# Kernel tuning notes

Hardware: AMD Instinct MI355X
Metric: run time of the kernel (lower is better)

## Reference

```python
import jax, jax.numpy as jnp
import numpy as np

B, S, D, H, F = 2, 4096, 768, 12, 3072
DK = D // H
EPS = 1e-5


def _layernorm(x, alpha, gamma):
    # Faithful to the custom Layernormalization: torch.std (unbiased, ddof=1),
    # (x - mean) / (std + eps), scalar alpha/gamma.
    m = jnp.mean(x, axis=-1, keepdims=True)
    s = jnp.std(x, axis=-1, ddof=1, keepdims=True)
    return alpha * ((x - m) / (s + EPS)) + gamma


def setup_inputs() -> dict:
    key = jax.random.key(0)
    ks = jax.random.split(key, 12)
    sc = 0.02
    inp = {
        "x": jax.random.normal(ks[0], (B, S, D), jnp.float32),
        # attention projections, stored as [in, out]
        "wq": jax.random.normal(ks[1], (D, D), jnp.float32) * sc,
        "bq": jnp.zeros((D,), jnp.float32),
        "wk": jax.random.normal(ks[2], (D, D), jnp.float32) * sc,
        "bk": jnp.zeros((D,), jnp.float32),
        "wv": jax.random.normal(ks[3], (D, D), jnp.float32) * sc,
        "bv": jnp.zeros((D,), jnp.float32),
        "wo": jax.random.normal(ks[4], (D, D), jnp.float32) * sc,
        "bo": jnp.zeros((D,), jnp.float32),
        # feedforward
        "w1": jax.random.normal(ks[5], (D, F), jnp.float32) * sc,
        "b1": jnp.zeros((F,), jnp.float32),
        "w2": jax.random.normal(ks[6], (F, D), jnp.float32) * sc,
        "b2": jnp.zeros((D,), jnp.float32),
        # two residual LayerNorms, scalar params (alpha=1, gamma=0 at init)
        "a1": jnp.ones((1,), jnp.float32),
        "g1": jnp.zeros((1,), jnp.float32),
        "a2": jnp.ones((1,), jnp.float32),
        "g2": jnp.zeros((1,), jnp.float32),
    }
    return inp


def reference(x, wq, bq, wk, bk, wv, bv, wo, bo, w1, b1, w2, b2, a1, g1, a2, g2):
    # --- self attention sublayer ---
    q = (x @ wq + bq).reshape(B, S, H, DK).transpose(0, 2, 1, 3)  # [B,H,S,dk]
    k = (x @ wk + bk).reshape(B, S, H, DK).transpose(0, 2, 1, 3)
    v = (x @ wv + bv).reshape(B, S, H, DK).transpose(0, 2, 1, 3)
    scores = jnp.einsum("bhqd,bhkd->bhqk", q, k) / np.sqrt(DK).astype(np.float32)
    attn = jax.nn.softmax(scores, axis=-1)  # dropout is identity (p=0 / eval)
    ctx = jnp.einsum("bhqk,bhkd->bhqd", attn, v)  # [B,H,S,dk]
    ctx = ctx.transpose(0, 2, 1, 3).reshape(B, S, D)
    attn_out = ctx @ wo + bo
    x = _layernorm(x + attn_out, a1, g1)
    # --- feedforward sublayer ---
    ff = jax.nn.relu(x @ w1 + b1) @ w2 + b2
    x = _layernorm(x + ff, a2, g2)
    return x
```

## Files before the change

kernel.cpp:

```cpp
#include <hip/hip_runtime.h>
#include <hip/hip_bf16.h>
#include <cstdint>
#include <cstddef>

typedef unsigned short u16;
typedef __attribute__((ext_vector_type(8))) __bf16 bf16x8;
typedef __attribute__((ext_vector_type(4))) float f32x4;

#define AS1 __attribute__((address_space(1)))
#define AS3 __attribute__((address_space(3)))

__device__ __forceinline__ u16 f2bf(float f) {
    union { float f; uint32_t u; } v; v.f = f;
    uint32_t r = (v.u + 0x7FFFu + ((v.u >> 16) & 1u)) >> 16;
    return (u16)r;
}

__device__ __forceinline__ float bf2f(u16 b) {
    union { uint32_t u; float f; } v; v.u = ((uint32_t)b) << 16;
    return v.f;
}

__device__ __forceinline__ uint32_t pack_bf2(float lo, float hi) {
    __hip_bfloat162 p = __float22bfloat162_rn(float2{lo, hi});
    union { __hip_bfloat162 b; uint32_t u; } v; v.b = p;
    return v.u;
}

__device__ __forceinline__ f32x4 mfma16(bf16x8 a, bf16x8 b, f32x4 c) {
    return __builtin_amdgcn_mfma_f32_16x16x32_bf16(a, b, c, 0, 0, 0);
}

__device__ __forceinline__ void async16(const u16* g, u16* lds_uniform_base) {
    __builtin_amdgcn_global_load_lds((const AS1 void*)g, (AS3 void*)lds_uniform_base, 16, 0, 0);
}

__global__ __launch_bounds__(256)
void k_prep(const float* __restrict__ x, u16* __restrict__ xb,
            const float* __restrict__ wq, const float* __restrict__ wk,
            const float* __restrict__ wv, const float* __restrict__ wo,
            const float* __restrict__ w1, const float* __restrict__ w2,
            u16* __restrict__ wqkvt, u16* __restrict__ wot,
            u16* __restrict__ w1t, u16* __restrict__ w2t)
{
    int bx = blockIdx.x;
    if (bx < 6144) {
        int i = (bx * 256 + threadIdx.x) * 4;
        float4 f = *(const float4*)(x + i);
        xb[i + 0] = f2bf(f.x); xb[i + 1] = f2bf(f.y);
        xb[i + 2] = f2bf(f.z); xb[i + 3] = f2bf(f.w);
        return;
    }
    int t = bx - 6144;
    const float* in; u16* out; int R, C;
    if (t < 2304) {
        int m = t / 576; t -= m * 576;
        R = 768; C = 768;
        in = (m == 0) ? wq : (m == 1) ? wk : (m == 2) ? wv : wo;
        out = (m < 3) ? wqkvt + (size_t)m * 768 * 768 : wot;
    } else if (t < 4608) {
        t -= 2304; in = w1; out = w1t; R = 768; C = 3072;
    } else {
        t -= 4608; in = w2; out = w2t; R = 3072; C = 768;
    }
    int tilesX = C >> 5;
    int c0 = (t % tilesX) * 32, r0 = (t / tilesX) * 32;
    __shared__ float tile[32][33];
    int tx = threadIdx.x & 31, ty = threadIdx.x >> 5;
    #pragma unroll
    for (int i = ty; i < 32; i += 8)
        tile[i][tx] = in[(size_t)(r0 + i) * C + c0 + tx];
    __syncthreads();
    #pragma unroll
    for (int i = ty; i < 32; i += 8)
        out[(size_t)(c0 + i) * R + r0 + tx] = f2bf(tile[tx][i]);
}

template <bool RELU>
__global__ __launch_bounds__(256)
void k_gemm(const u16* __restrict__ A, const u16* __restrict__ Bt,
            const float* __restrict__ bias, u16* __restrict__ Cb,
            int M, int N, int K)
{
    __shared__ __align__(16) u16 lA[128 * 32];
    __shared__ __align__(16) u16 lB[128 * 32];
    const int tid = threadIdx.x;
    const int w = tid >> 6, lane = tid & 63;
    const int quad = lane >> 4, l15 = lane & 15;
    const int m0 = blockIdx.x * 128, n0 = blockIdx.y * 128;
    const int wm = (w >> 1) * 64, wn = (w & 1) * 64;
    const int sw = (quad ^ ((l15 >> 1) & 3)) * 8;

    const f32x4 fz = {0.f, 0.f, 0.f, 0.f};
    f32x4 acc[4][4];
    #pragma unroll
    for (int i = 0; i < 4; ++i)
        #pragma unroll
        for (int j = 0; j < 4; ++j) acc[i][j] = fz;

    for (int k0 = 0; k0 < K; k0 += 32) {
        #pragma unroll
        for (int r = 0; r < 2; ++r) {
            int c = r * 256 + tid;
            int row = c >> 2, ch = (c & 3) ^ ((row >> 1) & 3);
            async16(A + (size_t)(m0 + row) * K + k0 + ch * 8,
                    (u16*)lA + (size_t)(r * 256 + w * 64) * 8);
            async16(Bt + (size_t)(n0 + row) * K + k0 + ch * 8,
                    (u16*)lB + (size_t)(r * 256 + w * 64) * 8);
        }
        __syncthreads();
        bf16x8 af[4], bfr[4];
        #pragma unroll
        for (int i = 0; i < 4; ++i)
            af[i] = *(const bf16x8*)&lA[(wm + i * 16 + l15) * 32 + sw];
        #pragma unroll
        for (int j = 0; j < 4; ++j)
            bfr[j] = *(const bf16x8*)&lB[(wn + j * 16 + l15) * 32 + sw];
        #pragma unroll
        for (int i = 0; i < 4; ++i)
            #pragma unroll
            for (int j = 0; j < 4; ++j)
                acc[i][j] = mfma16(af[i], bfr[j], acc[i][j]);
        __syncthreads();
    }
    #pragma unroll
    for (int j = 0; j < 4; ++j) {
        int col = n0 + wn + j * 16 + l15;
        float bv = bias[col];
        #pragma unroll
        for (int i = 0; i < 4; ++i) {
            int row = m0 + wm + i * 16 + quad * 4;
            #pragma unroll
            for (int r = 0; r < 4; ++r) {
                float t = acc[i][j][r] + bv;
                if (RELU) t = fmaxf(t, 0.f);
                Cb[(size_t)(row + r) * N + col] = f2bf(t);
            }
        }
    }
}

__global__ __launch_bounds__(256)
void k_gemm_part(const u16* __restrict__ A, const u16* __restrict__ Bt,
                 float* __restrict__ C0, float* __restrict__ C1,
                 int M, int N, int K, int Kh)
{
    __shared__ __align__(16) u16 lA[128 * 32];
    __shared__ __align__(16) u16 lB[128 * 32];
    const int tid = threadIdx.x;
    const int w = tid >> 6, lane = tid & 63;
    const int quad = lane >> 4, l15 = lane & 15;
    const int m0 = blockIdx.x * 128, n0 = blockIdx.y * 128;
    const int wm = (w >> 1) * 64, wn = (w & 1) * 64;
    const int sw = (quad ^ ((l15 >> 1) & 3)) * 8;
    const int kbeg = blockIdx.z * Kh, kend = kbeg + Kh;
    float* __restrict__ C = blockIdx.z ? C1 : C0;

    const f32x4 fz = {0.f, 0.f, 0.f, 0.f};
    f32x4 acc[4][4];
    #pragma unroll
    for (int i = 0; i < 4; ++i)
        #pragma unroll
        for (int j = 0; j < 4; ++j) acc[i][j] = fz;

    for (int k0 = kbeg; k0 < kend; k0 += 32) {
        #pragma unroll
        for (int r = 0; r < 2; ++r) {
            int c = r * 256 + tid;
            int row = c >> 2, ch = (c & 3) ^ ((row >> 1) & 3);
            async16(A + (size_t)(m0 + row) * K + k0 + ch * 8,
                    (u16*)lA + (size_t)(r * 256 + w * 64) * 8);
            async16(Bt + (size_t)(n0 + row) * K + k0 + ch * 8,
                    (u16*)lB + (size_t)(r * 256 + w * 64) * 8);
        }
        __syncthreads();
        bf16x8 af[4], bfr[4];
        #pragma unroll
        for (int i = 0; i < 4; ++i)
            af[i] = *(const bf16x8*)&lA[(wm + i * 16 + l15) * 32 + sw];
        #pragma unroll
        for (int j = 0; j < 4; ++j)
            bfr[j] = *(const bf16x8*)&lB[(wn + j * 16 + l15) * 32 + sw];
        #pragma unroll
        for (int i = 0; i < 4; ++i)
            #pragma unroll
            for (int j = 0; j < 4; ++j)
                acc[i][j] = mfma16(af[i], bfr[j], acc[i][j]);
        __syncthreads();
    }
    #pragma unroll
    for (int j = 0; j < 4; ++j) {
        int col = n0 + wn + j * 16 + l15;
        #pragma unroll
        for (int i = 0; i < 4; ++i) {
            int row = m0 + wm + i * 16 + quad * 4;
            #pragma unroll
            for (int r = 0; r < 4; ++r)
                C[(size_t)(row + r) * N + col] = acc[i][j][r];
        }
    }
}

__global__ __launch_bounds__(256)
void k_gemm_qkv(const u16* __restrict__ A, const u16* __restrict__ Bt,
                const float* __restrict__ bq, const float* __restrict__ bk,
                const float* __restrict__ bv,
                u16* __restrict__ qb, u16* __restrict__ kb, u16* __restrict__ vtg,
                int M, int K, float scale_q)
{
    __shared__ __align__(16) u16 qsm[4 * 64 * 72];
    u16* lA = qsm;
    u16* lB = qsm + 4096;
    const int tid = threadIdx.x;
    const int w = tid >> 6, lane = tid & 63;
    const int quad = lane >> 4, l15 = lane & 15;
    const int m0 = blockIdx.x * 128, n0 = blockIdx.y * 128;
    const int wm = (w >> 1) * 64, wn = (w & 1) * 64;
    const int sw = (quad ^ ((l15 >> 1) & 3)) * 8;
    const int sel = blockIdx.y / 6;
    const int cl0 = n0 - sel * 768;

    const f32x4 fz = {0.f, 0.f, 0.f, 0.f};
    f32x4 acc[4][4];
    #pragma unroll
    for (int i = 0; i < 4; ++i)
        #pragma unroll
        for (int j = 0; j < 4; ++j) acc[i][j] = fz;

    for (int k0 = 0; k0 < K; k0 += 32) {
        #pragma unroll
        for (int r = 0; r < 2; ++r) {
            int c = r * 256 + tid;
            int row = c >> 2, ch = (c & 3) ^ ((row >> 1) & 3);
            async16(A + (size_t)(m0 + row) * K + k0 + ch * 8,
                    lA + (size_t)(r * 256 + w * 64) * 8);
            async16(Bt + (size_t)(n0 + row) * K + k0 + ch * 8,
                    lB + (size_t)(r * 256 + w * 64) * 8);
        }
        __syncthreads();
        bf16x8 af[4], bfr[4];
        #pragma unroll
        for (int i = 0; i < 4; ++i)
            af[i] = *(const bf16x8*)&lA[(wm + i * 16 + l15) * 32 + sw];
        #pragma unroll
        for (int j = 0; j < 4; ++j)
            bfr[j] = *(const bf16x8*)&lB[(wn + j * 16 + l15) * 32 + sw];
        #pragma unroll
        for (int i = 0; i < 4; ++i)
            #pragma unroll
            for (int j = 0; j < 4; ++j)
                acc[i][j] = mfma16(af[i], bfr[j], acc[i][j]);
        __syncthreads();
    }
    const float* bias = (sel == 0) ? bq : (sel == 1) ? bk : bv;
    if (sel < 2) {
        u16* out = (sel == 0) ? qb : kb;
        float sc = (sel == 0) ? scale_q : 1.f;
        #pragma unroll
        for (int j = 0; j < 4; ++j) {
            int cl = cl0 + wn + j * 16 + l15;
            float bvv = bias[cl];
            #pragma unroll
            for (int i = 0; i < 4; ++i) {
                int row = m0 + wm + i * 16 + quad * 4;
                #pragma unroll
                for (int r = 0; r < 4; ++r)
                    out[(size_t)(row + r) * 768 + cl] = f2bf((acc[i][j][r] + bvv) * sc);
            }
        }
    } else {
        u16* lT = qsm + w * 4608;
        #pragma unroll
        for (int j = 0; j < 4; ++j) {
            float bvv = bias[cl0 + wn + j * 16 + l15];
            #pragma unroll
            for (int i = 0; i < 4; ++i)
                #pragma unroll
                for (int r = 0; r < 4; ++r)
                    lT[(j * 16 + l15) * 72 + i * 16 + quad * 4 + r]
                        = f2bf(acc[i][j][r] + bvv);
        }
        int gcol = cl0 + wn + lane;
        u16* gdst = vtg + (size_t)gcol * M + m0 + wm;
        #pragma unroll
        for (int kk = 0; kk < 8; ++kk) {
            bf16x8 v = *(const bf16x8*)&lT[lane * 72 + kk * 8];
            *(bf16x8*)(gdst + kk * 8) = v;
        }
    }
}

__global__ __launch_bounds__(256, 3)
void k_attention(const u16* __restrict__ Q, const u16* __restrict__ Kb,
                 const u16* __restrict__ Vt, u16* __restrict__ ctx,
                 int S, int D, int H, int M)
{
    __shared__ __align__(16) u16 sKV[16384];
    __shared__ __align__(16) u16 sP[4608];
    __shared__ float sL[2][64];
    const int qt = blockIdx.x, bh = blockIdx.y;
    const int b = bh / H, h = bh % H;
    const int tid = threadIdx.x, w = tid >> 6, lane = tid & 63;
    const int wq = w & 1, wk = w >> 1;
    const int quad = lane >> 4, l15 = lane & 15;
    const int sw = (quad ^ ((l15 >> 1) & 3)) * 8;
    const size_t bS = (size_t)b * S;
    const int q0 = qt * 128 + wq * 64;

    bf16x8 qf[4][2];
    #pragma unroll
    for (int set = 0; set < 4; ++set)
        #pragma unroll
        for (int kc = 0; kc < 2; ++kc)
            qf[set][kc] = *(const bf16x8*)(Q + (bS + q0 + set * 16 + l15) * D
                                           + (size_t)h * 64 + kc * 32 + quad * 8);

    const f32x4 fz = {0.f, 0.f, 0.f, 0.f};
    f32x4 O[4][4];
    #pragma unroll
    for (int s = 0; s < 4; ++s)
        #pragma unroll
        for (int j = 0; j < 4; ++j) O[s][j] = fz;
    float l_[4] = {0.f, 0.f, 0.f, 0.f};
    u16* myP = sP + w * 1152;

    const u16* kbase = Kb + bS * D + (size_t)h * 64;
    const u16* vbase = Vt + (size_t)h * 64 * M + bS;

    const u16* gk[2]; const u16* gv[2];
    #pragma unroll
    for (int i = 0; i < 2; ++i) {
        int c = i * 256 + tid;
        int kc = c >> 8;
        int krow = (c >> 2) & 63, kch = (c & 3) ^ ((krow >> 1) & 3);
        gk[i] = kbase + (size_t)krow * D + kc * 32 + kch * 8;
        int dk = (c >> 2) & 63, vch = (c & 3) ^ ((dk >> 1) & 3);
        gv[i] = vbase + (size_t)dk * M + kc * 32 + vch * 8;
    }
    const int dslot = (w * 64) * 8;

    #pragma unroll
    for (int i = 0; i < 2; ++i) {
        async16(gk[i], sKV + i * 2048 + dslot);
        async16(gv[i], sKV + 8192 + i * 2048 + dslot);
        gk[i] += (size_t)64 * D;
        gv[i] += 64;
    }

    const int T = S >> 6;
    for (int t = 0; t < T; ++t) {
        __syncthreads();
        if (t + 1 < T) {
            int nb = (t + 1) & 1;
            #pragma unroll
            for (int i = 0; i < 2; ++i) {
                async16(gk[i], sKV + nb * 4096 + i * 2048 + dslot);
                async16(gv[i], sKV + 8192 + nb * 4096 + i * 2048 + dslot);
                gk[i] += (size_t)64 * D;
                gv[i] += 64;
            }
        }
        const u16* lKb = sKV + (t & 1) * 4096;
        const u16* lVb = sKV + 8192 + (t & 1) * 4096;

        bf16x8 ka[2][2], vf[4];
        #pragma unroll
        for (int ks = 0; ks < 2; ++ks)
            #pragma unroll
            for (int kc = 0; kc < 2; ++kc)
                ka[ks][kc] = *(const bf16x8*)
                    &lKb[kc * 2048 + (wk * 32 + ks * 16 + l15) * 32 + sw];
        #pragma unroll
        for (int dj = 0; dj < 4; ++dj)
            vf[dj] = *(const bf16x8*)
                &lVb[wk * 2048 + (dj * 16 + l15) * 32 + sw];

        #pragma unroll
        for (int set = 0; set < 4; ++set) {
            f32x4 sc0 = fz, sc1 = fz;
            sc0 = mfma16(ka[0][0], qf[set][0], sc0);
            sc0 = mfma16(ka[0][1], qf[set][1], sc0);
            sc1 = mfma16(ka[1][0], qf[set][0], sc1);
            sc1 = mfma16(ka[1][1], qf[set][1], sc1);
            float p0[4], p1[4];
            float rs = 0.f;
            #pragma unroll
            for (int r = 0; r < 4; ++r) {
                p0[r] = __builtin_amdgcn_exp2f(sc0[r]);
                p1[r] = __builtin_amdgcn_exp2f(sc1[r]);
                rs += p0[r] + p1[r];
            }
            l_[set] += rs;
            uint2 d0, d1;
            d0.x = pack_bf2(p0[0], p0[1]); d0.y = pack_bf2(p0[2], p0[3]);
            d1.x = pack_bf2(p1[0], p1[1]); d1.y = pack_bf2(p1[2], p1[3]);
            u16* Pb = myP + (set & 1) * 576;
            *(uint2*)&Pb[l15 * 36 + quad * 4] = d0;
            *(uint2*)&Pb[l15 * 36 + 16 + quad * 4] = d1;
            bf16x8 pa = *(const bf16x8*)&Pb[l15 * 36 + quad * 8];
            #pragma unroll
            for (int dj = 0; dj < 4; ++dj)
                O[set][dj] = mfma16(pa, vf[dj], O[set][dj]);
        }
    }

    float lred[4];
    #pragma unroll
    for (int set = 0; set < 4; ++set) {
        float lt = l_[set];
        lt += __shfl_xor(lt, 16, 64);
        lt += __shfl_xor(lt, 32, 64);
        lred[set] = lt;
    }
    __syncthreads();
    u16* lO = sKV;
    if (wk == 1) {
        #pragma unroll
        for (int set = 0; set < 4; ++set) {
            #pragma unroll
            for (int dj = 0; dj < 4; ++dj)
                #pragma unroll
                for (int r = 0; r < 4; ++r)
                    lO[(wq * 64 + set * 16 + quad * 4 + r) * 66 + dj * 16 + l15]
                        = f2bf(O[set][dj][r]);
            if (lane < 16) sL[wq][set * 16 + lane] = lred[set];
        }
    }
    __syncthreads();
    if (wk == 0) {
        #pragma unroll
        for (int set = 0; set < 4; ++set) {
            float ltot = lred[set] + sL[wq][set * 16 + l15];
            float rl[4];
            #pragma unroll
            for (int r = 0; r < 4; ++r)
                rl[r] = 1.f / __shfl(ltot, quad * 4 + r, 64);
            #pragma unroll
            for (int dj = 0; dj < 4; ++dj)
                #pragma unroll
                for (int r = 0; r < 4; ++r) {
                    float o = O[set][dj][r]
                        + bf2f(lO[(wq * 64 + set * 16 + quad * 4 + r) * 66 + dj * 16 + l15]);
                    ctx[(bS + q0 + set * 16 + quad * 4 + r) * D
                        + (size_t)h * 64 + dj * 16 + l15] = f2bf(o * rl[r]);
                }
        }
    }
}

__global__ __launch_bounds__(256)
void k_layernorm2(const float* __restrict__ p0, const float* __restrict__ p1,
                  const float* __restrict__ resid, const float* __restrict__ bias,
                  const float* __restrict__ a, const float* __restrict__ g,
                  float* __restrict__ outf, u16* __restrict__ outb, int D)
{
    const int row = blockIdx.x, tid = threadIdx.x;
    const size_t base = (size_t)row * D;
    float v[3];
    float s = 0.f, sq = 0.f;
    #pragma unroll
    for (int i = 0; i < 3; ++i) {
        int c = tid + i * 256;
        float x = p0[base + c] + p1[base + c] + resid[base + c] + bias[c];
        v[i] = x; s += x; sq += x * x;
    }
    #pragma unroll
    for (int off = 32; off >= 1; off >>= 1) {
        s += __shfl_xor(s, off, 64);
        sq += __shfl_xor(sq, off, 64);
    }
    __shared__ float red[8];
    const int w = tid >> 6;
    if ((tid & 63) == 0) { red[w] = s; red[4 + w] = sq; }
    __syncthreads();
    s = red[0] + red[1] + red[2] + red[3];
    sq = red[4] + red[5] + red[6] + red[7];
    float mean = s / D;
    float var = fmaxf((sq - s * mean) / (D - 1), 0.f);
    float denom = sqrtf(var) + 1e-5f;
    float av = a[0], gv = g[0];
    #pragma unroll
    for (int i = 0; i < 3; ++i) {
        float y = av * ((v[i] - mean) / denom) + gv;
        if (outf) outf[base + tid + i * 256] = y;
        if (outb) outb[base + tid + i * 256] = f2bf(y);
    }
}

extern "C" void kernel_launch(void* const* d_in, const int* in_sizes, int n_in,
                              void* d_out, int out_size, void* d_ws, size_t ws_size,
                              hipStream_t stream)
{
    constexpr int B = 2, S = 4096, D = 768, H = 12, F = 3072;
    constexpr int M = B * S;
    const float SCALE_Q = 1.4426950408889634f / 8.0f;
    const float* x  = (const float*)d_in[0];
    const float* wq = (const float*)d_in[1];
    const float* bq = (const float*)d_in[2];
    const float* wk = (const float*)d_in[3];
    const float* bk = (const float*)d_in[4];
    const float* wv = (const float*)d_in[5];
    const float* bv = (const float*)d_in[6];
    const float* wo = (const float*)d_in[7];
    const float* bo = (const float*)d_in[8];
    const float* w1 = (const float*)d_in[9];
    const float* b1 = (const float*)d_in[10];
    const float* w2 = (const float*)d_in[11];
    const float* b2 = (const float*)d_in[12];
    const float* a1 = (const float*)d_in[13];
    const float* g1 = (const float*)d_in[14];
    const float* a2 = (const float*)d_in[15];
    const float* g2 = (const float*)d_in[16];

    char* ws = (char*)d_ws;
    size_t off = 0;
    auto alloc = [&](size_t bytes) {
        void* p = ws + off;
        off = (off + bytes + 255) & ~(size_t)255;
        return p;
    };
    u16*   xb    = (u16*)alloc((size_t)M * D * 2);
    u16*   wqkvt = (u16*)alloc((size_t)3 * D * D * 2);
    u16*   wot   = (u16*)alloc((size_t)D * D * 2);
    u16*   w1t   = (u16*)alloc((size_t)D * F * 2);
    u16*   w2t   = (u16*)alloc((size_t)D * F * 2);
    u16*   qb    = (u16*)alloc((size_t)M * D * 2);
    u16*   kb    = (u16*)alloc((size_t)M * D * 2);
    u16*   vtg   = (u16*)alloc((size_t)M * D * 2);
    u16*   ctxb  = (u16*)alloc((size_t)M * D * 2);
    float* x1f   = (float*)alloc((size_t)M * D * 4);
    u16*   x1b   = (u16*)alloc((size_t)M * D * 2);
    u16*   ff1b  = (u16*)alloc((size_t)M * F * 2);

    float* p0a = (float*)qb;
    float* p1a = (float*)ff1b;
    float* p0b = (float*)qb;
    float* p1b = (float*)vtg;

    k_prep<<<6144 + 6912, 256, 0, stream>>>(x, xb, wq, wk, wv, wo, w1, w2,
                                            wqkvt, wot, w1t, w2t);

    k_gemm_qkv<<<dim3(M / 128, 3 * D / 128), 256, 0, stream>>>(
        xb, wqkvt, bq, bk, bv, qb, kb, vtg, M, D, SCALE_Q);

    k_attention<<<dim3(S / 128, B * H), 256, 0, stream>>>(qb, kb, vtg, ctxb, S, D, H, M);

    k_gemm_part<<<dim3(M / 128, D / 128, 2), 256, 0, stream>>>(
        ctxb, wot, p0a, p1a, M, D, D, D / 2);
    k_layernorm2<<<M, 256, 0, stream>>>(p0a, p1a, x, bo, a1, g1, x1f, x1b, D);

    k_gemm<true><<<dim3(M / 128, F / 128), 256, 0, stream>>>(
        x1b, w1t, b1, ff1b, M, F, D);
    k_gemm_part<<<dim3(M / 128, D / 128, 2), 256, 0, stream>>>(
        ff1b, w2t, p0b, p1b, M, D, F, F / 2);
    k_layernorm2<<<M, 256, 0, stream>>>(p0b, p1b, x1f, b2, a2, g2, (float*)d_out, nullptr, D);

    (void)in_sizes; (void)n_in; (void)out_size; (void)ws_size;
}
```

Before: 508.2 us.

## Split attention block across eight waves with 32 query rows each and MFMA priority hints

The attention kernel moves from 256 to 512 threads per block. Each wave now handles 32 query rows instead of 64, which halves the per-wave Q fragments, output accumulators and row sums. The K/V tile load is spread so each thread issues one async copy per operand instead of two, and s_setprio hints are wrapped around the MFMA groups to favour matrix issue. The aim is lower register pressure and more waves in flight to hide latency, at the cost of more LDS for P buffers and more per-tile fragment reloads across waves.

```diff
diff --git a/kernel.cpp b/kernel.cpp
--- a/kernel.cpp
+++ b/kernel.cpp
@@ -290,75 +290,65 @@
     }
 }
 
-__global__ __launch_bounds__(256, 3)
+__global__ __launch_bounds__(512, 4)
 void k_attention(const u16* __restrict__ Q, const u16* __restrict__ Kb,
                  const u16* __restrict__ Vt, u16* __restrict__ ctx,
                  int S, int D, int H, int M)
 {
     __shared__ __align__(16) u16 sKV[16384];
-    __shared__ __align__(16) u16 sP[4608];
-    __shared__ float sL[2][64];
+    __shared__ __align__(16) u16 sP[9216];
+    __shared__ float sL[4][32];
     const int qt = blockIdx.x, bh = blockIdx.y;
     const int b = bh / H, h = bh % H;
     const int tid = threadIdx.x, w = tid >> 6, lane = tid & 63;
-    const int wq = w & 1, wk = w >> 1;
+    const int wq = w & 3, wk = w >> 2;
     const int quad = lane >> 4, l15 = lane & 15;
     const int sw = (quad ^ ((l15 >> 1) & 3)) * 8;
     const size_t bS = (size_t)b * S;
-    const int q0 = qt * 128 + wq * 64;
-
-    bf16x8 qf[4][2];
-    #pragma unroll
-    for (int set = 0; set < 4; ++set)
+    const int q0 = qt * 128 + wq * 32;
+
+    bf16x8 qf[2][2];
+    #pragma unroll
+    for (int set = 0; set < 2; ++set)
         #pragma unroll
         for (int kc = 0; kc < 2; ++kc)
             qf[set][kc] = *(const bf16x8*)(Q + (bS + q0 + set * 16 + l15) * D
                                            + (size_t)h * 64 + kc * 32 + quad * 8);
 
     const f32x4 fz = {0.f, 0.f, 0.f, 0.f};
-    f32x4 O[4][4];
-    #pragma unroll
-    for (int s = 0; s < 4; ++s)
+    f32x4 O[2][4];
+    #pragma unroll
+    for (int s = 0; s < 2; ++s)
         #pragma unroll
         for (int j = 0; j < 4; ++j) O[s][j] = fz;
-    float l_[4] = {0.f, 0.f, 0.f, 0.f};
+    float l_[2] = {0.f, 0.f};
     u16* myP = sP + w * 1152;
 
     const u16* kbase = Kb + bS * D + (size_t)h * 64;
     const u16* vbase = Vt + (size_t)h * 64 * M + bS;
 
-    const u16* gk[2]; const u16* gv[2];
-    #pragma unroll
-    for (int i = 0; i < 2; ++i) {
-        int c = i * 256 + tid;
-        int kc = c >> 8;
-        int krow = (c >> 2) & 63, kch = (c & 3) ^ ((krow >> 1) & 3);
-        gk[i] = kbase + (size_t)krow * D + kc * 32 + kch * 8;
-        int dk = (c >> 2) & 63, vch = (c & 3) ^ ((dk >> 1) & 3);
-        gv[i] = vbase + (size_t)dk * M + kc * 32 + vch * 8;
-    }
-    const int dslot = (w * 64) * 8;
-
-    #pragma unroll
-    for (int i = 0; i < 2; ++i) {
-        async16(gk[i], sKV + i * 2048 + dslot);
-        async16(gv[i], sKV + 8192 + i * 2048 + dslot);
-        gk[i] += (size_t)64 * D;
-        gv[i] += 64;
-    }
+    const int c = tid;
+    const int kc_ = c >> 8;
+    const int krow = (c >> 2) & 63, kch = (c & 3) ^ ((krow >> 1) & 3);
+    const u16* gk = kbase + (size_t)krow * D + kc_ * 32 + kch * 8;
+    const int vdk = (c >> 2) & 63, vch = (c & 3) ^ ((vdk >> 1) & 3);
+    const u16* gv = vbase + (size_t)vdk * M + kc_ * 32 + vch * 8;
+    const int dslot = w * 512;
+
+    async16(gk, sKV + dslot);
+    async16(gv, sKV + 8192 + dslot);
+    gk += (size_t)64 * D;
+    gv += 64;
 
     const int T = S >> 6;
     for (int t = 0; t < T; ++t) {
         __syncthreads();
         if (t + 1 < T) {
             int nb = (t + 1) & 1;
-            #pragma unroll
-            for (int i = 0; i < 2; ++i) {
-                async16(gk[i], sKV + nb * 4096 + i * 2048 + dslot);
-                async16(gv[i], sKV + 8192 + nb * 4096 + i * 2048 + dslot);
-                gk[i] += (size_t)64 * D;
-                gv[i] += 64;
-            }
+            async16(gk, sKV + nb * 4096 + dslot);
+            async16(gv, sKV + 8192 + nb * 4096 + dslot);
+            gk += (size_t)64 * D;
+            gv += 64;
         }
         const u16* lKb = sKV + (t & 1) * 4096;
         const u16* lVb = sKV + 8192 + (t & 1) * 4096;
@@ -376,12 +366,14 @@
                 &lVb[wk * 2048 + (dj * 16 + l15) * 32 + sw];
 
         #pragma unroll
-        for (int set = 0; set < 4; ++set) {
+        for (int set = 0; set < 2; ++set) {
             f32x4 sc0 = fz, sc1 = fz;
+            __builtin_amdgcn_s_setprio(1);
             sc0 = mfma16(ka[0][0], qf[set][0], sc0);
             sc0 = mfma16(ka[0][1], qf[set][1], sc0);
             sc1 = mfma16(ka[1][0], qf[set][0], sc1);
             sc1 = mfma16(ka[1][1], qf[set][1], sc1);
+            __builtin_amdgcn_s_setprio(0);
             float p0[4], p1[4];
             float rs = 0.f;
             #pragma unroll
@@ -394,19 +386,21 @@
             uint2 d0, d1;
             d0.x = pack_bf2(p0[0], p0[1]); d0.y = pack_bf2(p0[2], p0[3]);
             d1.x = pack_bf2(p1[0], p1[1]); d1.y = pack_bf2(p1[2], p1[3]);
-            u16* Pb = myP + (set & 1) * 576;
+            u16* Pb = myP + set * 576;
             *(uint2*)&Pb[l15 * 36 + quad * 4] = d0;
             *(uint2*)&Pb[l15 * 36 + 16 + quad * 4] = d1;
             bf16x8 pa = *(const bf16x8*)&Pb[l15 * 36 + quad * 8];
+            __builtin_amdgcn_s_setprio(1);
             #pragma unroll
             for (int dj = 0; dj < 4; ++dj)
                 O[set][dj] = mfma16(pa, vf[dj], O[set][dj]);
-        }
-    }
-
-    float lred[4];
-    #pragma unroll
-    for (int set = 0; set < 4; ++set) {
+            __builtin_amdgcn_s_setprio(0);
+        }
+    }
+
+    float lred[2];
+    #pragma unroll
+    for (int set = 0; set < 2; ++set) {
         float lt = l_[set];
         lt += __shfl_xor(lt, 16, 64);
         lt += __shfl_xor(lt, 32, 64);
@@ -416,12 +410,12 @@
     u16* lO = sKV;
     if (wk == 1) {
         #pragma unroll
-        for (int set = 0; set < 4; ++set) {
+        for (int set = 0; set < 2; ++set) {
             #pragma unroll
             for (int dj = 0; dj < 4; ++dj)
                 #pragma unroll
                 for (int r = 0; r < 4; ++r)
-                    lO[(wq * 64 + set * 16 + quad * 4 + r) * 66 + dj * 16 + l15]
+                    lO[(wq * 32 + set * 16 + quad * 4 + r) * 66 + dj * 16 + l15]
                         = f2bf(O[set][dj][r]);
             if (lane < 16) sL[wq][set * 16 + lane] = lred[set];
         }
@@ -429,7 +423,7 @@
     __syncthreads();
     if (wk == 0) {
         #pragma unroll
-        for (int set = 0; set < 4; ++set) {
+        for (int set = 0; set < 2; ++set) {
             float ltot = lred[set] + sL[wq][set * 16 + l15];
             float rl[4];
             #pragma unroll
@@ -440,7 +434,7 @@
                 #pragma unroll
                 for (int r = 0; r < 4; ++r) {
                     float o = O[set][dj][r]
-                        + bf2f(lO[(wq * 64 + set * 16 + quad * 4 + r) * 66 + dj * 16 + l15]);
+                        + bf2f(lO[(wq * 32 + set * 16 + quad * 4 + r) * 66 + dj * 16 + l15]);
                     ctx[(bS + q0 + set * 16 + quad * 4 + r) * D
                         + (size_t)h * 64 + dj * 16 + l15] = f2bf(o * rl[r]);
                 }
@@ -543,7 +537,7 @@
     k_gemm_qkv<<<dim3(M / 128, 3 * D / 128), 256, 0, stream>>>(
         xb, wqkvt, bq, bk, bv, qb, kb, vtg, M, D, SCALE_Q);
 
-    k_attention<<<dim3(S / 128, B * H), 256, 0, stream>>>(qb, kb, vtg, ctxb, S, D, H, M);
+    k_attention<<<dim3(S / 128, B * H), 512, 0, stream>>>(qb, kb, vtg, ctxb, S, D, H, M);
 
     k_gemm_part<<<dim3(M / 128, D / 128, 2), 256, 0, stream>>>(
         ctxb, wot, p0a, p1a, M, D, D, D / 2);
```

New measurement: 530.5 us. 1.04x slower.
